# Kernel optimization log

Hardware: AMD Instinct MI355X
Metric: run time of the kernel (lower is better)

## Reference

```python
import jax, jax.numpy as jnp
import numpy as np

B, L, D = 4096, 50, 128          # users, neighbors/user, embed_dim
N_U, N_I, N_R, N_T = 10000, 100000, 6, 1000
EPS = 1e-5                       # BatchNorm eps (eval mode, running stats)


def setup_inputs() -> dict:
    key = jax.random.key(0)
    ks = iter(jax.random.split(key, 80))
    nk = lambda: next(ks)

    def lin(din, dout):
        s = 1.0 / np.sqrt(din)
        w = jax.random.uniform(nk(), (din, dout), minval=-s, maxval=s, dtype=jnp.float32)
        b = jax.random.uniform(nk(), (dout,), minval=-s, maxval=s, dtype=jnp.float32)
        return w, b

    inp = {}
    # embedding tables (u2e/i2e/r2e/t2e)
    inp['u2e'] = 0.1 * jax.random.normal(nk(), (N_U, D), jnp.float32)
    inp['i2e'] = 0.1 * jax.random.normal(nk(), (N_I, D), jnp.float32)
    inp['r2e'] = 0.1 * jax.random.normal(nk(), (N_R, D), jnp.float32)
    inp['t2e'] = 0.1 * jax.random.normal(nk(), (N_T, D), jnp.float32)
    # neighbor transform MLP
    inp['ne_w'], inp['ne_b'] = lin(3 * D, D)
    inp['ne1_w'], inp['ne1_b'] = lin(D, D)
    # attention MLP (NewAttention: concat(neigh, user) -> D -> D -> 1, softmax over neighbors)
    inp['att1_w'], inp['att1_b'] = lin(2 * D, D)
    inp['att2_w'], inp['att2_b'] = lin(D, D)
    inp['att3_w'], inp['att3_b'] = lin(D, 1)
    # head
    inp['lin_w'], inp['lin_b'] = lin(2 * D, D)
    inp['w1_w'], inp['w1_b'] = lin(D, D // 4)
    inp['bn1_g'] = jnp.ones((D // 4,), jnp.float32)
    inp['bn1_b'] = jnp.zeros((D // 4,), jnp.float32)
    inp['bn1_m'] = 0.1 * jax.random.normal(nk(), (D // 4,), jnp.float32)
    inp['bn1_v'] = jax.random.uniform(nk(), (D // 4,), minval=0.5, maxval=1.5, dtype=jnp.float32)
    inp['w2_w'], inp['w2_b'] = lin(D // 4, D // 8)
    inp['bn2_g'] = jnp.ones((D // 8,), jnp.float32)
    inp['bn2_b'] = jnp.zeros((D // 8,), jnp.float32)
    inp['bn2_m'] = 0.1 * jax.random.normal(nk(), (D // 8,), jnp.float32)
    inp['bn2_v'] = jax.random.uniform(nk(), (D // 8,), minval=0.5, maxval=1.5, dtype=jnp.float32)
    inp['w3_w'], inp['w3_b'] = lin(D // 8, 1)
    # index inputs (padded-fixed neighbor lists)
    inp['user_idx'] = jax.random.randint(nk(), (B,), 0, N_U)
    inp['item_idx'] = jax.random.randint(nk(), (B, L), 0, N_I)
    inp['rat_idx'] = jax.random.randint(nk(), (B, L), 0, N_R)
    inp['time_idx'] = jax.random.randint(nk(), (B, L), 0, N_T)
    return inp


def reference(u2e, i2e, r2e, t2e, ne_w, ne_b, ne1_w, ne1_b,
              att1_w, att1_b, att2_w, att2_b, att3_w, att3_b,
              lin_w, lin_b, w1_w, w1_b, bn1_g, bn1_b, bn1_m, bn1_v,
              w2_w, w2_b, bn2_g, bn2_b, bn2_m, bn2_v, w3_w, w3_b,
              user_idx, item_idx, rat_idx, time_idx):
    u = u2e[user_idx]                                                   # [B, D]
    neigh = jnp.concatenate([i2e[item_idx], r2e[rat_idx], t2e[time_idx]], axis=-1)  # [B, L, 3D]
    x = jax.nn.relu(neigh @ ne_w + ne_b)                                # [B, L, D]
    x = jax.nn.relu(x @ ne1_w + ne1_b)                                  # [B, L, D]
    # attention over neighbors, conditioned on the user embedding
    a = jnp.concatenate([x, jnp.broadcast_to(u[:, None, :], x.shape)], axis=-1)  # [B, L, 2D]
    a = jax.nn.relu(a @ att1_w + att1_b)
    a = jax.nn.relu(a @ att2_w + att2_b)
    att = jax.nn.softmax((a @ att3_w + att3_b)[..., 0], axis=-1)        # [B, L]
    pooled = jnp.einsum('bl,bld->bd', att, x)                           # torch.mm(x.t(), att).t()
    comb = jax.nn.relu(jnp.concatenate([u, pooled], axis=-1) @ lin_w + lin_b)  # [B, D]
    h = comb @ w1_w + w1_b
    h = jax.nn.relu((h - bn1_m) * jax.lax.rsqrt(bn1_v + EPS) * bn1_g + bn1_b)
    h = h @ w2_w + w2_b
    h = jax.nn.relu((h - bn2_m) * jax.lax.rsqrt(bn2_v + EPS) * bn2_g + bn2_b)
    return (h @ w3_w + w3_b)[:, 0]                                      # [B]
```

## Files before the change

kernel.cpp:

```cpp
#include <hip/hip_runtime.h>
#include <hip/hip_bf16.h>

typedef __bf16 bf16x8 __attribute__((ext_vector_type(8)));
typedef float  f32x4  __attribute__((ext_vector_type(4)));

#define W_OFF 0
#define A_OFF 32768
#define B_OFF 46080
#define X_OFF 59392
#define SMALL 72704
#define SMEM_TOTAL 76736
#define WCHUNK 16384

__global__ void prep_weights_kernel(const float* __restrict__ ne_w,
                                    const float* __restrict__ ne1_w,
                                    const float* __restrict__ att1_w,
                                    const float* __restrict__ att2_w,
                                    __hip_bfloat16* __restrict__ wout) {
  __shared__ float tile[64][65];
  const int bx = blockIdx.x;
  const int c = bx >> 2, kt = (bx >> 1) & 1, ntile = bx & 1;
  const float* src; int koff;
  if      (c < 3)  { src = ne_w;   koff = c * 128; }
  else if (c == 3) { src = ne1_w;  koff = 0; }
  else if (c == 4) { src = att1_w; koff = 0; }
  else             { src = att2_w; koff = 0; }
  const int tx = threadIdx.x, ty = threadIdx.y;
#pragma unroll
  for (int r = 0; r < 16; ++r) {
    int k = kt * 64 + r * 4 + ty, n = ntile * 64 + tx;
    tile[r * 4 + ty][tx] = src[(koff + k) * 128 + n];
  }
  __syncthreads();
#pragma unroll
  for (int r = 0; r < 16; ++r) {
    int n = ntile * 64 + r * 4 + ty, k = kt * 64 + tx;
    int off = (c * 128 + n) * 128 + (((k >> 3) ^ (n & 15)) << 3) + (k & 7);
    wout[off] = __float2bfloat16(tile[tx][r * 4 + ty]);
  }
}

__device__ __forceinline__ unsigned short bf_bits(float x) {
  return __builtin_bit_cast(unsigned short, __float2bfloat16(x));
}

__device__ __forceinline__ void mfma_chunk(const __hip_bfloat16* sIn,
                                           const __hip_bfloat16* sWl,
                                           f32x4 acc[4], int m16, int nh, int lane) {
  const int mr = lane & 15;
  const int kq = lane >> 4;
  const int arow = (m16 * 16 + mr) * 128;
#pragma unroll
  for (int ks = 0; ks < 4; ++ks) {
    const int swz = (((ks * 4 + kq) ^ mr) << 3);
    bf16x8 a = *(const bf16x8*)(sIn + arow + swz);
#pragma unroll
    for (int nt = 0; nt < 4; ++nt) {
      const int n = nh * 64 + nt * 16 + mr;
      bf16x8 b = *(const bf16x8*)(sWl + n * 128 + swz);
      acc[nt] = __builtin_amdgcn_mfma_f32_16x16x32_bf16(a, b, acc[nt], 0, 0, 0);
    }
  }
}

__device__ __forceinline__ void epilogue(f32x4 acc[4], const float* __restrict__ bias,
                                         const float* addvec, __hip_bfloat16* sOut,
                                         int m16, int nh, int lane) {
  const int mr = lane & 15;
  const int rb = m16 * 16 + ((lane >> 4) << 2);
#pragma unroll
  for (int nt = 0; nt < 4; ++nt) {
    const int col = nh * 64 + nt * 16 + mr;
    float bv = bias[col];
    if (addvec) bv += addvec[col];
    const int cblk = col >> 3, clo = col & 7;
#pragma unroll
    for (int r = 0; r < 4; ++r) {
      const int row = rb + r;
      if (row < 50) {
        float v = fmaxf(acc[nt][r] + bv, 0.0f);
        sOut[row * 128 + ((cblk ^ (row & 15)) << 3) + clo] = __float2bfloat16(v);
      }
    }
  }
}

__global__ __launch_bounds__(512, 4) void graphdec_main(
    const float* __restrict__ u2e, const float* __restrict__ i2e,
    const float* __restrict__ r2e, const float* __restrict__ t2e,
    const float* __restrict__ ne_b, const float* __restrict__ ne1_b,
    const float* __restrict__ att1_w, const float* __restrict__ att1_b,
    const float* __restrict__ att3_w, const float* __restrict__ att3_b,
    const float* __restrict__ att2_b,
    const float* __restrict__ lin_w, const float* __restrict__ lin_b,
    const float* __restrict__ w1_w, const float* __restrict__ w1_b,
    const float* __restrict__ bn1_g, const float* __restrict__ bn1_b,
    const float* __restrict__ bn1_m, const float* __restrict__ bn1_v,
    const float* __restrict__ w2_w, const float* __restrict__ w2_b,
    const float* __restrict__ bn2_g, const float* __restrict__ bn2_b,
    const float* __restrict__ bn2_m, const float* __restrict__ bn2_v,
    const float* __restrict__ w3_w, const float* __restrict__ w3_b,
    const int* __restrict__ user_idx, const int* __restrict__ item_idx,
    const int* __restrict__ rat_idx, const int* __restrict__ time_idx,
    const __hip_bfloat16* __restrict__ wprep, float* __restrict__ out) {
  __shared__ __align__(16) unsigned char smem[SMEM_TOTAL];
  __hip_bfloat16* sW = (__hip_bfloat16*)(smem + W_OFF);
  __hip_bfloat16* sA = (__hip_bfloat16*)(smem + A_OFF);
  __hip_bfloat16* sB = (__hip_bfloat16*)(smem + B_OFF);
  __hip_bfloat16* sX = (__hip_bfloat16*)(smem + X_OFF);
  float* sUf    = (float*)(smem + SMALL);
  float* sAtt3  = (float*)(smem + SMALL + 512);
  int*   sIdx   = (int*)  (smem + SMALL + 1024);
  float* sUatt  = (float*)(smem + SMALL + 1792);
  float* sLogit = (float*)(smem + SMALL + 2304);
  float* sAtt   = (float*)(smem + SMALL + 2560);
  float* sPooled= (float*)(smem + SMALL + 2816);
  float* sComb  = (float*)(smem + SMALL + 3328);
  float* sH1    = (float*)(smem + SMALL + 3840);
  float* sUatt4 = (float*)(smem + X_OFF);
  float* sPool4 = (float*)(smem + W_OFF);
  float* sCombP = (float*)(smem + W_OFF + 2048);

  const int tid  = threadIdx.x;
  const int lane = tid & 63;
  const int wid  = tid >> 6;
  const int m16  = wid & 3;
  const int nh   = wid >> 2;
  const int b    = blockIdx.x;

  if (tid < 192) {
    int c = tid >> 6, l = tid & 63;
    int v = 0;
    if (l < 50) {
      const int* p = (c == 0) ? item_idx : (c == 1) ? rat_idx : time_idx;
      v = p[b * 50 + l];
    }
    sIdx[tid] = v;
  } else if (tid < 320) {
    sAtt3[tid - 192] = att3_w[tid - 192];
  } else if (tid < 448) {
    sUf[tid - 320] = u2e[user_idx[b] * 128 + (tid - 320)];
  }
  __syncthreads();

  auto gather = [&](int c, const float* __restrict__ tab, __hip_bfloat16* dst) {
    const float4* t4 = (const float4*)tab;
#pragma unroll
    for (int i = 0; i < 2; ++i) {
      int g = tid + i * 512;
      if (g < 832) {
        int row = g >> 4, kb = g & 15;
        float4 v0 = {0.f,0.f,0.f,0.f}, v1 = {0.f,0.f,0.f,0.f};
        if (row < 50) {
          long base = (long)sIdx[c * 64 + row] * 32 + kb * 2;
          v0 = t4[base]; v1 = t4[base + 1];
        }
        uint4 pk;
        pk.x = ((unsigned)bf_bits(v0.y) << 16) | bf_bits(v0.x);
        pk.y = ((unsigned)bf_bits(v0.w) << 16) | bf_bits(v0.z);
        pk.z = ((unsigned)bf_bits(v1.y) << 16) | bf_bits(v1.x);
        pk.w = ((unsigned)bf_bits(v1.w) << 16) | bf_bits(v1.z);
        *(uint4*)(dst + row * 128 + ((kb ^ (row & 15)) << 3)) = pk;
      }
    }
  };

  auto stage = [&](const __hip_bfloat16* __restrict__ src) {
#pragma unroll
    for (int i = 0; i < 4; ++i) {
      int g = tid + i * 512;
      __builtin_amdgcn_global_load_lds(
          (__attribute__((address_space(1))) void*)(void*)(src + g * 8),
          (__attribute__((address_space(3))) void*)(void*)(sW + g * 8), 16, 0, 0);
    }
  };

  f32x4 acc[4];
  const f32x4 zf = {0.f, 0.f, 0.f, 0.f};
  auto zacc = [&]() {
#pragma unroll
    for (int j = 0; j < 4; ++j) acc[j] = zf;
  };

  gather(0, i2e, sA);
  stage(wprep + 0 * WCHUNK);
  {
    int q = tid >> 7, d = tid & 127;
    float s = 0.f;
    for (int k = q * 32; k < q * 32 + 32; ++k) s += sUf[k] * att1_w[(128 + k) * 128 + d];
    sUatt4[q * 128 + d] = s;
  }
  __syncthreads();

  zacc();
  mfma_chunk(sA, sW, acc, m16, nh, lane);
  gather(1, r2e, sB);
  if (tid < 128)
    sUatt[tid] = sUatt4[tid] + sUatt4[128 + tid] + sUatt4[256 + tid] + sUatt4[384 + tid];
  __syncthreads();
  stage(wprep + 1 * WCHUNK);
  gather(2, t2e, sA);
  __syncthreads();
  mfma_chunk(sB, sW, acc, m16, nh, lane);
  __syncthreads();
  stage(wprep + 2 * WCHUNK);
  __syncthreads();
  mfma_chunk(sA, sW, acc, m16, nh, lane);
  epilogue(acc, ne_b, nullptr, sB, m16, nh, lane);
  __syncthreads();

  stage(wprep + 3 * WCHUNK);
  __syncthreads();
  zacc();
  mfma_chunk(sB, sW, acc, m16, nh, lane);
  epilogue(acc, ne1_b, nullptr, sX, m16, nh, lane);
  __syncthreads();

  stage(wprep + 4 * WCHUNK);
  __syncthreads();
  zacc();
  mfma_chunk(sX, sW, acc, m16, nh, lane);
  epilogue(acc, att1_b, sUatt, sA, m16, nh, lane);
  __syncthreads();

  stage(wprep + 5 * WCHUNK);
  __syncthreads();
  zacc();
  mfma_chunk(sA, sW, acc, m16, nh, lane);
  epilogue(acc, att2_b, nullptr, sB, m16, nh, lane);
  __syncthreads();

  {
    int row = tid >> 3, p = tid & 7;
    const int base = row * 128;
    bf16x8 b0 = *(const bf16x8*)(sB + base + (((2 * p) ^ (row & 15)) << 3));
    bf16x8 b1 = *(const bf16x8*)(sB + base + (((2 * p + 1) ^ (row & 15)) << 3));
    float s = 0.f;
#pragma unroll
    for (int j = 0; j < 8; ++j) {
      s += (float)b0[j] * sAtt3[p * 16 + j];
      s += (float)b1[j] * sAtt3[p * 16 + 8 + j];
    }
    s += __shfl_xor(s, 1); s += __shfl_xor(s, 2); s += __shfl_xor(s, 4);
    if (p == 0) sLogit[row] = s + att3_b[0];
  }
  __syncthreads();

  if (wid == 0) {
    float v = (lane < 50) ? sLogit[lane] : -3.4e38f;
    float m = v;
    for (int off = 32; off > 0; off >>= 1) m = fmaxf(m, __shfl_xor(m, off));
    float e = (lane < 50) ? __expf(v - m) : 0.f;
    float s = e;
    for (int off = 32; off > 0; off >>= 1) s += __shfl_xor(s, off);
    sAtt[lane] = e / s;
  }
  __syncthreads();

  {
    int q = tid >> 7, d = tid & 127;
    const int cblk = d >> 3, clo = d & 7;
    float s = 0.f;
    for (int l = q; l < 50; l += 4)
      s += sAtt[l] * (float)sX[l * 128 + ((cblk ^ (l & 15)) << 3) + clo];
    sPool4[q * 128 + d] = s;
  }
  __syncthreads();
  if (tid < 128)
    sPooled[tid] = sPool4[tid] + sPool4[128 + tid] + sPool4[256 + tid] + sPool4[384 + tid];
  __syncthreads();

  {
    int q = tid >> 7, d = tid & 127;
    const float* inb = (q < 2) ? (sUf + q * 64) : (sPooled + (q - 2) * 64);
    const int base = q * 64;
    float s = 0.f;
    for (int j = 0; j < 64; ++j) s += inb[j] * lin_w[(base + j) * 128 + d];
    sCombP[q * 128 + d] = s;
  }
  __syncthreads();
  if (tid < 128)
    sComb[tid] = fmaxf(sCombP[tid] + sCombP[128 + tid] + sCombP[256 + tid] + sCombP[384 + tid]
                       + lin_b[tid], 0.f);
  __syncthreads();

  if (wid == 0) {
    if (lane < 32) {
      float s = w1_b[lane];
      for (int k = 0; k < 128; ++k) s += sComb[k] * w1_w[k * 32 + lane];
      s = (s - bn1_m[lane]) * rsqrtf(bn1_v[lane] + 1e-5f) * bn1_g[lane] + bn1_b[lane];
      sH1[lane] = fmaxf(s, 0.f);
    }
    if (lane < 16) {
      float s = w2_b[lane];
      for (int k = 0; k < 32; ++k) s += sH1[k] * w2_w[k * 16 + lane];
      s = (s - bn2_m[lane]) * rsqrtf(bn2_v[lane] + 1e-5f) * bn2_g[lane] + bn2_b[lane];
      float p = fmaxf(s, 0.f) * w3_w[lane];
      p += __shfl_xor(p, 1); p += __shfl_xor(p, 2);
      p += __shfl_xor(p, 4); p += __shfl_xor(p, 8);
      if (lane == 0) out[b] = p + w3_b[0];
    }
  }
}

extern "C" void kernel_launch(void* const* d_in, const int* in_sizes, int n_in,
                              void* d_out, int out_size, void* d_ws, size_t ws_size,
                              hipStream_t stream) {
  const float* u2e    = (const float*)d_in[0];
  const float* i2e    = (const float*)d_in[1];
  const float* r2e    = (const float*)d_in[2];
  const float* t2e    = (const float*)d_in[3];
  const float* ne_w   = (const float*)d_in[4];
  const float* ne_b   = (const float*)d_in[5];
  const float* ne1_w  = (const float*)d_in[6];
  const float* ne1_b  = (const float*)d_in[7];
  const float* att1_w = (const float*)d_in[8];
  const float* att1_b = (const float*)d_in[9];
  const float* att2_w = (const float*)d_in[10];
  const float* att2_b = (const float*)d_in[11];
  const float* att3_w = (const float*)d_in[12];
  const float* att3_b = (const float*)d_in[13];
  const float* lin_w  = (const float*)d_in[14];
  const float* lin_b  = (const float*)d_in[15];
  const float* w1_w   = (const float*)d_in[16];
  const float* w1_b   = (const float*)d_in[17];
  const float* bn1_g  = (const float*)d_in[18];
  const float* bn1_b  = (const float*)d_in[19];
  const float* bn1_m  = (const float*)d_in[20];
  const float* bn1_v  = (const float*)d_in[21];
  const float* w2_w   = (const float*)d_in[22];
  const float* w2_b   = (const float*)d_in[23];
  const float* bn2_g  = (const float*)d_in[24];
  const float* bn2_b  = (const float*)d_in[25];
  const float* bn2_m  = (const float*)d_in[26];
  const float* bn2_v  = (const float*)d_in[27];
  const float* w3_w   = (const float*)d_in[28];
  const float* w3_b   = (const float*)d_in[29];
  const int* user_idx = (const int*)d_in[30];
  const int* item_idx = (const int*)d_in[31];
  const int* rat_idx  = (const int*)d_in[32];
  const int* time_idx = (const int*)d_in[33];
  __hip_bfloat16* wprep = (__hip_bfloat16*)d_ws;
  float* out = (float*)d_out;

  prep_weights_kernel<<<24, dim3(64, 4), 0, stream>>>(ne_w, ne1_w, att1_w, att2_w, wprep);
  graphdec_main<<<4096, 512, 0, stream>>>(
      u2e, i2e, r2e, t2e, ne_b, ne1_b, att1_w, att1_b, att3_w, att3_b, att2_b,
      lin_w, lin_b, w1_w, w1_b, bn1_g, bn1_b, bn1_m, bn1_v, w2_w, w2_b,
      bn2_g, bn2_b, bn2_m, bn2_v, w3_w, w3_b,
      user_idx, item_idx, rat_idx, time_idx, wprep, out);
}
```

Measured before the change: 300.1 us.

## Precompute per-table first-layer projections and user projections before the main kernel

Uses the linearity of the first neighbor layer and of the user halves of att1 and lin. Two new pre-pass kernels project the full item, rating and time tables through their ne_w chunks, and the user table through the att1 and lin user blocks, into workspace every call. The main kernel then gathers the projected rows, sums them with bias and ReLU, and skips three MFMA chunks plus the per-block user matvecs. In exchange it adds a dense GEMM over all 100k items and a scalar fp32 pass over all 10k users, along with roughly 100MB of extra workspace traffic per call.

```diff
diff --git a/kernel.cpp b/kernel.cpp
--- a/kernel.cpp
+++ b/kernel.cpp
@@ -11,6 +11,13 @@
 #define SMALL 72704
 #define SMEM_TOTAL 76736
 #define WCHUNK 16384
+
+#define WS_WPREP 0
+#define WS_PI    196608
+#define WS_PT    (WS_PI + 51200000)
+#define WS_PR    (WS_PT + 512000)
+#define WS_PU    (WS_PR + 3072)
+#define WS_PU2   (WS_PU + 5120000)
 
 __global__ void prep_weights_kernel(const float* __restrict__ ne_w,
                                     const float* __restrict__ ne1_w,
@@ -85,11 +92,91 @@
   }
 }
 
+__global__ __launch_bounds__(512) void pgemm_kernel(
+    const float* __restrict__ i2e, const float* __restrict__ r2e,
+    const float* __restrict__ t2e, const __hip_bfloat16* __restrict__ wprep,
+    float* __restrict__ Pi, float* __restrict__ Pt, float* __restrict__ Pr) {
+  __shared__ __align__(16) __hip_bfloat16 sW[WCHUNK];
+  __shared__ __align__(16) __hip_bfloat16 sA[64 * 128];
+  const int tid = threadIdx.x, lane = tid & 63, wid = tid >> 6;
+  const int m16 = wid & 3, nh = wid >> 2;
+  const int bx = blockIdx.x;
+  const float* src; const __hip_bfloat16* W; float* dst; long rows0; int nrows;
+  if (bx < 1563)      { src = i2e; W = wprep + 0 * WCHUNK; dst = Pi; rows0 = (long)bx * 64;          nrows = 100000; }
+  else if (bx < 1579) { src = t2e; W = wprep + 2 * WCHUNK; dst = Pt; rows0 = (long)(bx - 1563) * 64; nrows = 1000; }
+  else                { src = r2e; W = wprep + 1 * WCHUNK; dst = Pr; rows0 = 0;                      nrows = 6; }
+
+#pragma unroll
+  for (int i = 0; i < 4; ++i) {
+    int g = tid + i * 512;
+    __builtin_amdgcn_global_load_lds(
+        (__attribute__((address_space(1))) void*)(void*)(W + g * 8),
+        (__attribute__((address_space(3))) void*)(void*)(sW + g * 8), 16, 0, 0);
+  }
+  const float4* s4 = (const float4*)src;
+#pragma unroll
+  for (int i = 0; i < 2; ++i) {
+    int g = tid + i * 512;
+    int row = g >> 4, kb = g & 15;
+    float4 v0 = {0.f, 0.f, 0.f, 0.f}, v1 = {0.f, 0.f, 0.f, 0.f};
+    if (rows0 + row < nrows) {
+      long base = (rows0 + row) * 32 + kb * 2;
+      v0 = s4[base]; v1 = s4[base + 1];
+    }
+    uint4 pk;
+    pk.x = ((unsigned)bf_bits(v0.y) << 16) | bf_bits(v0.x);
+    pk.y = ((unsigned)bf_bits(v0.w) << 16) | bf_bits(v0.z);
+    pk.z = ((unsigned)bf_bits(v1.y) << 16) | bf_bits(v1.x);
+    pk.w = ((unsigned)bf_bits(v1.w) << 16) | bf_bits(v1.z);
+    *(uint4*)(sA + row * 128 + ((kb ^ (row & 15)) << 3)) = pk;
+  }
+  __syncthreads();
+
+  f32x4 acc[4];
+#pragma unroll
+  for (int j = 0; j < 4; ++j) acc[j] = (f32x4){0.f, 0.f, 0.f, 0.f};
+  mfma_chunk(sA, sW, acc, m16, nh, lane);
+
+  const int mr = lane & 15;
+  const int rb = m16 * 16 + ((lane >> 4) << 2);
+#pragma unroll
+  for (int nt = 0; nt < 4; ++nt) {
+    const int col = nh * 64 + nt * 16 + mr;
+#pragma unroll
+    for (int r = 0; r < 4; ++r) {
+      const int row = rb + r;
+      if (rows0 + row < nrows) dst[(rows0 + row) * 128 + col] = acc[nt][r];
+    }
+  }
+}
+
+__global__ __launch_bounds__(256) void pu_kernel(const float* __restrict__ u2e,
+                                                 const float* __restrict__ att1_w,
+                                                 const float* __restrict__ lin_w,
+                                                 float* __restrict__ Pu,
+                                                 float* __restrict__ Pu2) {
+  int idx = blockIdx.x * 256 + threadIdx.x;
+  const int HALF = 10000 * 128;
+  bool second = idx >= HALF;
+  if (second) idx -= HALF;
+  int u = idx >> 7, d = idx & 127;
+  const float* urow = u2e + (long)u * 128;
+  float s = 0.f;
+  if (!second) {
+    for (int k = 0; k < 128; ++k) s += urow[k] * att1_w[(128 + k) * 128 + d];
+    Pu[idx] = s;
+  } else {
+    for (int k = 0; k < 128; ++k) s += urow[k] * lin_w[k * 128 + d];
+    Pu2[idx] = s;
+  }
+}
+
 __global__ __launch_bounds__(512, 4) void graphdec_main(
-    const float* __restrict__ u2e, const float* __restrict__ i2e,
-    const float* __restrict__ r2e, const float* __restrict__ t2e,
+    const float* __restrict__ Pi, const float* __restrict__ Pt,
+    const float* __restrict__ Pr, const float* __restrict__ Pu,
+    const float* __restrict__ Pu2,
     const float* __restrict__ ne_b, const float* __restrict__ ne1_b,
-    const float* __restrict__ att1_w, const float* __restrict__ att1_b,
+    const float* __restrict__ att1_b,
     const float* __restrict__ att3_w, const float* __restrict__ att3_b,
     const float* __restrict__ att2_b,
     const float* __restrict__ lin_w, const float* __restrict__ lin_b,
@@ -108,16 +195,15 @@
   __hip_bfloat16* sA = (__hip_bfloat16*)(smem + A_OFF);
   __hip_bfloat16* sB = (__hip_bfloat16*)(smem + B_OFF);
   __hip_bfloat16* sX = (__hip_bfloat16*)(smem + X_OFF);
-  float* sUf    = (float*)(smem + SMALL);
-  float* sAtt3  = (float*)(smem + SMALL + 512);
-  int*   sIdx   = (int*)  (smem + SMALL + 1024);
-  float* sUatt  = (float*)(smem + SMALL + 1792);
+  float* sAtt3  = (float*)(smem + SMALL);
+  int*   sIdx   = (int*)  (smem + SMALL + 512);
+  float* sUatt  = (float*)(smem + SMALL + 1280);
+  float* sUlin  = (float*)(smem + SMALL + 1792);
   float* sLogit = (float*)(smem + SMALL + 2304);
   float* sAtt   = (float*)(smem + SMALL + 2560);
   float* sPooled= (float*)(smem + SMALL + 2816);
   float* sComb  = (float*)(smem + SMALL + 3328);
   float* sH1    = (float*)(smem + SMALL + 3840);
-  float* sUatt4 = (float*)(smem + X_OFF);
   float* sPool4 = (float*)(smem + W_OFF);
   float* sCombP = (float*)(smem + W_OFF + 2048);
 
@@ -138,32 +224,11 @@
     sIdx[tid] = v;
   } else if (tid < 320) {
     sAtt3[tid - 192] = att3_w[tid - 192];
-  } else if (tid < 448) {
-    sUf[tid - 320] = u2e[user_idx[b] * 128 + (tid - 320)];
-  }
-  __syncthreads();
-
-  auto gather = [&](int c, const float* __restrict__ tab, __hip_bfloat16* dst) {
-    const float4* t4 = (const float4*)tab;
-#pragma unroll
-    for (int i = 0; i < 2; ++i) {
-      int g = tid + i * 512;
-      if (g < 832) {
-        int row = g >> 4, kb = g & 15;
-        float4 v0 = {0.f,0.f,0.f,0.f}, v1 = {0.f,0.f,0.f,0.f};
-        if (row < 50) {
-          long base = (long)sIdx[c * 64 + row] * 32 + kb * 2;
-          v0 = t4[base]; v1 = t4[base + 1];
-        }
-        uint4 pk;
-        pk.x = ((unsigned)bf_bits(v0.y) << 16) | bf_bits(v0.x);
-        pk.y = ((unsigned)bf_bits(v0.w) << 16) | bf_bits(v0.z);
-        pk.z = ((unsigned)bf_bits(v1.y) << 16) | bf_bits(v1.x);
-        pk.w = ((unsigned)bf_bits(v1.w) << 16) | bf_bits(v1.z);
-        *(uint4*)(dst + row * 128 + ((kb ^ (row & 15)) << 3)) = pk;
-      }
-    }
-  };
+  }
+  const int uid = user_idx[b];
+  if (tid < 128)      sUatt[tid]       = Pu [(long)uid * 128 + tid];
+  else if (tid < 256) sUlin[tid - 128] = Pu2[(long)uid * 128 + (tid - 128)];
+  __syncthreads();
 
   auto stage = [&](const __hip_bfloat16* __restrict__ src) {
 #pragma unroll
@@ -182,59 +247,63 @@
     for (int j = 0; j < 4; ++j) acc[j] = zf;
   };
 
-  gather(0, i2e, sA);
-  stage(wprep + 0 * WCHUNK);
-  {
-    int q = tid >> 7, d = tid & 127;
-    float s = 0.f;
-    for (int k = q * 32; k < q * 32 + 32; ++k) s += sUf[k] * att1_w[(128 + k) * 128 + d];
-    sUatt4[q * 128 + d] = s;
+  stage(wprep + 3 * WCHUNK);
+#pragma unroll
+  for (int i = 0; i < 2; ++i) {
+    int g = tid + i * 512;
+    if (g < 832) {
+      int row = g >> 4, kb = g & 15;
+      uint4 pk = {0u, 0u, 0u, 0u};
+      if (row < 50) {
+        const float4* pi4 = (const float4*)(Pi + (long)sIdx[row] * 128) + kb * 2;
+        const float4* pr4 = (const float4*)(Pr + (long)sIdx[64 + row] * 128) + kb * 2;
+        const float4* pt4 = (const float4*)(Pt + (long)sIdx[128 + row] * 128) + kb * 2;
+        float4 a0 = pi4[0], a1 = pi4[1];
+        float4 r0 = pr4[0], r1 = pr4[1];
+        float4 t0 = pt4[0], t1 = pt4[1];
+        const float* nb = ne_b + kb * 8;
+        float s0 = fmaxf(a0.x + r0.x + t0.x + nb[0], 0.f);
+        float s1 = fmaxf(a0.y + r0.y + t0.y + nb[1], 0.f);
+        float s2 = fmaxf(a0.z + r0.z + t0.z + nb[2], 0.f);
+        float s3 = fmaxf(a0.w + r0.w + t0.w + nb[3], 0.f);
+        float s4 = fmaxf(a1.x + r1.x + t1.x + nb[4], 0.f);
+        float s5 = fmaxf(a1.y + r1.y + t1.y + nb[5], 0.f);
+        float s6 = fmaxf(a1.z + r1.z + t1.z + nb[6], 0.f);
+        float s7 = fmaxf(a1.w + r1.w + t1.w + nb[7], 0.f);
+        pk.x = ((unsigned)bf_bits(s1) << 16) | bf_bits(s0);
+        pk.y = ((unsigned)bf_bits(s3) << 16) | bf_bits(s2);
+        pk.z = ((unsigned)bf_bits(s5) << 16) | bf_bits(s4);
+        pk.w = ((unsigned)bf_bits(s7) << 16) | bf_bits(s6);
+      }
+      *(uint4*)(sA + row * 128 + ((kb ^ (row & 15)) << 3)) = pk;
+    }
   }
   __syncthreads();
 
   zacc();
   mfma_chunk(sA, sW, acc, m16, nh, lane);
-  gather(1, r2e, sB);
-  if (tid < 128)
-    sUatt[tid] = sUatt4[tid] + sUatt4[128 + tid] + sUatt4[256 + tid] + sUatt4[384 + tid];
-  __syncthreads();
-  stage(wprep + 1 * WCHUNK);
-  gather(2, t2e, sA);
-  __syncthreads();
-  mfma_chunk(sB, sW, acc, m16, nh, lane);
-  __syncthreads();
-  stage(wprep + 2 * WCHUNK);
-  __syncthreads();
-  mfma_chunk(sA, sW, acc, m16, nh, lane);
-  epilogue(acc, ne_b, nullptr, sB, m16, nh, lane);
-  __syncthreads();
-
-  stage(wprep + 3 * WCHUNK);
-  __syncthreads();
+  __syncthreads();
+  stage(wprep + 4 * WCHUNK);
+  epilogue(acc, ne1_b, nullptr, sX, m16, nh, lane);
+  __syncthreads();
+
+  zacc();
+  mfma_chunk(sX, sW, acc, m16, nh, lane);
+  __syncthreads();
+  stage(wprep + 5 * WCHUNK);
+  epilogue(acc, att1_b, sUatt, sB, m16, nh, lane);
+  __syncthreads();
+
   zacc();
   mfma_chunk(sB, sW, acc, m16, nh, lane);
-  epilogue(acc, ne1_b, nullptr, sX, m16, nh, lane);
-  __syncthreads();
-
-  stage(wprep + 4 * WCHUNK);
-  __syncthreads();
-  zacc();
-  mfma_chunk(sX, sW, acc, m16, nh, lane);
-  epilogue(acc, att1_b, sUatt, sA, m16, nh, lane);
-  __syncthreads();
-
-  stage(wprep + 5 * WCHUNK);
-  __syncthreads();
-  zacc();
-  mfma_chunk(sA, sW, acc, m16, nh, lane);
-  epilogue(acc, att2_b, nullptr, sB, m16, nh, lane);
+  epilogue(acc, att2_b, nullptr, sA, m16, nh, lane);
   __syncthreads();
 
   {
     int row = tid >> 3, p = tid & 7;
     const int base = row * 128;
-    bf16x8 b0 = *(const bf16x8*)(sB + base + (((2 * p) ^ (row & 15)) << 3));
-    bf16x8 b1 = *(const bf16x8*)(sB + base + (((2 * p + 1) ^ (row & 15)) << 3));
+    bf16x8 b0 = *(const bf16x8*)(sA + base + (((2 * p) ^ (row & 15)) << 3));
+    bf16x8 b1 = *(const bf16x8*)(sA + base + (((2 * p + 1) ^ (row & 15)) << 3));
     float s = 0.f;
 #pragma unroll
     for (int j = 0; j < 8; ++j) {
@@ -272,16 +341,14 @@
 
   {
     int q = tid >> 7, d = tid & 127;
-    const float* inb = (q < 2) ? (sUf + q * 64) : (sPooled + (q - 2) * 64);
-    const int base = q * 64;
     float s = 0.f;
-    for (int j = 0; j < 64; ++j) s += inb[j] * lin_w[(base + j) * 128 + d];
+    for (int j = q * 32; j < q * 32 + 32; ++j) s += sPooled[j] * lin_w[(128 + j) * 128 + d];
     sCombP[q * 128 + d] = s;
   }
   __syncthreads();
   if (tid < 128)
     sComb[tid] = fmaxf(sCombP[tid] + sCombP[128 + tid] + sCombP[256 + tid] + sCombP[384 + tid]
-                       + lin_b[tid], 0.f);
+                       + sUlin[tid] + lin_b[tid], 0.f);
   __syncthreads();
 
   if (wid == 0) {
@@ -340,12 +407,21 @@
   const int* item_idx = (const int*)d_in[31];
   const int* rat_idx  = (const int*)d_in[32];
   const int* time_idx = (const int*)d_in[33];
-  __hip_bfloat16* wprep = (__hip_bfloat16*)d_ws;
+
+  char* ws = (char*)d_ws;
+  __hip_bfloat16* wprep = (__hip_bfloat16*)(ws + WS_WPREP);
+  float* Pi  = (float*)(ws + WS_PI);
+  float* Pt  = (float*)(ws + WS_PT);
+  float* Pr  = (float*)(ws + WS_PR);
+  float* Pu  = (float*)(ws + WS_PU);
+  float* Pu2 = (float*)(ws + WS_PU2);
   float* out = (float*)d_out;
 
   prep_weights_kernel<<<24, dim3(64, 4), 0, stream>>>(ne_w, ne1_w, att1_w, att2_w, wprep);
+  pgemm_kernel<<<1580, 512, 0, stream>>>(i2e, r2e, t2e, wprep, Pi, Pt, Pr);
+  pu_kernel<<<10000, 256, 0, stream>>>(u2e, att1_w, lin_w, Pu, Pu2);
   graphdec_main<<<4096, 512, 0, stream>>>(
-      u2e, i2e, r2e, t2e, ne_b, ne1_b, att1_w, att1_b, att3_w, att3_b, att2_b,
+      Pi, Pt, Pr, Pu, Pu2, ne_b, ne1_b, att1_b, att3_w, att3_b, att2_b,
       lin_w, lin_b, w1_w, w1_b, bn1_g, bn1_b, bn1_m, bn1_v, w2_w, w2_b,
       bn2_g, bn2_b, bn2_m, bn2_v, w3_w, w3_b,
       user_idx, item_idx, rat_idx, time_idx, wprep, out);
```

Result: slower. 351.7 us (+17.2%).
